# Kernel tuning notes

Hardware: AMD Instinct MI355X
Metric: run time of the kernel (lower is better)

Reference implementation:

```python
import jax, jax.numpy as jnp
import numpy as np

NUM_HEADS = 16
ROPE_THETA = 10000.0


def _rope_tables(S, d_k):
    # angles[s, j] = s / theta^(2j/d_k), j over d_k/2 pairs
    inv_freq = 1.0 / (ROPE_THETA ** (jnp.arange(0, d_k, 2, dtype=jnp.float32) / d_k))
    angles = jnp.arange(S, dtype=jnp.float32)[:, None] * inv_freq[None, :]  # [S, d_k/2]
    # repeat_interleave(…, 2, dim=-1) -> [S, d_k]
    cos2 = jnp.repeat(jnp.cos(angles), 2, axis=-1)
    sin2 = jnp.repeat(jnp.sin(angles), 2, axis=-1)
    return cos2, sin2


def _rotate_half(x):
    x_even = x[..., 0::2]
    x_odd = x[..., 1::2]
    return jnp.stack([-x_odd, x_even], axis=-1).reshape(x.shape)


def _apply_rope(x, cos2, sin2):
    # x: [B, H, S, d_k]; cos2/sin2: [S, d_k] broadcast over B, H
    return x * cos2 + _rotate_half(x) * sin2


def setup_inputs() -> dict:
    key = jax.random.key(0)
    k1, k2, k3, k4, k5 = jax.random.split(key, 5)
    B, S, D = 2, 2048, 1024
    std = (2.0 / (D + D)) ** 0.5
    x = jax.random.normal(k1, (B, S, D), dtype=jnp.float32)
    Wq = jax.random.normal(k2, (D, D), dtype=jnp.float32) * std
    Wk = jax.random.normal(k3, (D, D), dtype=jnp.float32) * std
    Wv = jax.random.normal(k4, (D, D), dtype=jnp.float32) * std
    Wo = jax.random.normal(k5, (D, D), dtype=jnp.float32) * std
    return {"x": x, "Wq": Wq, "Wk": Wk, "Wv": Wv, "Wo": Wo}


def reference(x, Wq, Wk, Wv, Wo):
    B, S, D = x.shape
    H = NUM_HEADS
    d_k = D // H
    # Linear is y = W x with W[d_out, d_in]
    Q = jnp.einsum('bsd,ed->bse', x, Wq).reshape(B, S, H, d_k).transpose(0, 2, 1, 3)
    K = jnp.einsum('bsd,ed->bse', x, Wk).reshape(B, S, H, d_k).transpose(0, 2, 1, 3)
    V = jnp.einsum('bsd,ed->bse', x, Wv).reshape(B, S, H, d_k).transpose(0, 2, 1, 3)
    cos2, sin2 = _rope_tables(S, d_k)
    Q = _apply_rope(Q, cos2, sin2)
    K = _apply_rope(K, cos2, sin2)
    scores = jnp.einsum('bhqd,bhkd->bhqk', Q, K) / jnp.sqrt(jnp.float32(d_k))
    causal = jnp.tril(jnp.ones((S, S), dtype=bool))
    scores = jnp.where(causal, scores, -jnp.inf)
    attn = jax.nn.softmax(scores, axis=-1)
    out = jnp.einsum('bhqk,bhkd->bhqd', attn, V)  # [B,H,S,d_k]
    out = out.transpose(0, 2, 1, 3).reshape(B, S, D)
    return jnp.einsum('bsd,ed->bse', out, Wo)
```

## Files before the change

kernel.cpp:

```cpp
#include <hip/hip_runtime.h>
#include <hip/hip_bf16.h>

typedef float f32x4 __attribute__((ext_vector_type(4)));
typedef __bf16 bf16x8 __attribute__((ext_vector_type(8)));

static constexpr int S  = 2048;
static constexpr int D  = 1024;
static constexpr int DK = 64;
static constexpr int KDIM = 1024;

#define AS1 __attribute__((address_space(1)))
#define AS3 __attribute__((address_space(3)))

__device__ __forceinline__ void glds16(const void* g, void* l) {
  __builtin_amdgcn_global_load_lds((const AS1 void*)g, (AS3 void*)l, 16, 0, 0);
}

__device__ __forceinline__ unsigned cvtpk(float lo, float hi) {
  unsigned r;
  asm("v_cvt_pk_bf16_f32 %0, %1, %2" : "=v"(r) : "v"(lo), "v"(hi));
  return r;
}

__device__ __forceinline__ void pl32swap(unsigned& a, unsigned& b) {
  asm("v_permlane32_swap_b32 %0, %1" : "+v"(a), "+v"(b));
}

__device__ __forceinline__ int kperm64(int k) {
  const int kf = k >> 4, hs = (k >> 2) & 3, r = k & 3;
  const bool inl = ((kf & 1) == (hs >> 1));
  const int h = inl ? hs : (hs ^ 2);
  const int j = inl ? r : (r + 4);
  return ((kf >> 1) << 5) + (h << 3) + j;
}

__global__ __launch_bounds__(256) void pre_kernel(
    const float* __restrict__ x,  const float* __restrict__ Wq,
    const float* __restrict__ Wk, const float* __restrict__ Wv,
    const float* __restrict__ Wo,
    __hip_bfloat16* __restrict__ xb, __hip_bfloat16* __restrict__ Wcat,
    __hip_bfloat16* __restrict__ Wob,
    float* __restrict__ cosT, float* __restrict__ sinT) {
  const int gid = blockIdx.x * 256 + threadIdx.x;
  if (gid < 2097152) {
    const float* src;
    __hip_bfloat16* dst;
    int off;
    if (gid < 1048576)      { src = x;  dst = xb;                  off = gid; }
    else if (gid < 1310720) { src = Wq; dst = Wcat;                off = gid - 1048576; }
    else if (gid < 1572864) { src = Wk; dst = Wcat + 1048576;      off = gid - 1310720; }
    else if (gid < 1835008) { src = Wv; dst = Wcat + 2097152;      off = gid - 1572864; }
    else                    { src = Wo; dst = Wob;                 off = gid - 1835008; }
    float4 v = reinterpret_cast<const float4*>(src)[off];
    union { ushort4 u; __hip_bfloat16 h[4]; } o;
    o.h[0] = __float2bfloat16(v.x);
    o.h[1] = __float2bfloat16(v.y);
    o.h[2] = __float2bfloat16(v.z);
    o.h[3] = __float2bfloat16(v.w);
    reinterpret_cast<ushort4*>(dst)[off] = o.u;
  } else {
    const int idx = gid - 2097152;
    const int s = idx >> 5, fi = idx & 31;
    float invf = powf(10000.0f, -(float)(2 * fi) / 64.0f);
    float ang = (float)s * invf;
    cosT[idx] = cosf(ang);
    sinT[idx] = sinf(ang);
  }
}

template <int MODE>
__global__ __launch_bounds__(256) void gemm_nt_kernel(
    const __hip_bfloat16* __restrict__ A,
    const __hip_bfloat16* __restrict__ Bw,
    float* __restrict__ Cf,
    __hip_bfloat16* __restrict__ Qr,
    __hip_bfloat16* __restrict__ Kr,
    __hip_bfloat16* __restrict__ Vt,
    const float* __restrict__ cosT,
    const float* __restrict__ sinT,
    int Ncols) {
  __shared__ __attribute__((aligned(16))) __hip_bfloat16 Asm[128 * 32];
  __shared__ __attribute__((aligned(16))) __hip_bfloat16 Bsm[128 * 32];
  const int tid = threadIdx.x;
  const int nbn = Ncols >> 7;
  const int cpx = gridDim.x >> 3;
  const int swz = (blockIdx.x & 7) * cpx + (blockIdx.x >> 3);
  const int bm = swz / nbn;
  const int bn = swz % nbn;
  const int m0 = bm << 7, n0 = bn << 7;
  const int lane = tid & 63;
  const int wid = tid >> 6;
  const int wm = wid >> 1, wn = wid & 1;
  const int r16 = lane & 15, hf = lane >> 4;

  f32x4 acc[4][4];
#pragma unroll
  for (int i = 0; i < 4; ++i)
#pragma unroll
    for (int j = 0; j < 4; ++j) acc[i][j] = (f32x4)0.0f;

  for (int k0 = 0; k0 < KDIM; k0 += 32) {
    __syncthreads();
#pragma unroll
    for (int i = 0; i < 2; ++i) {
      const int idx = i * 256 + tid;
      const int row = idx >> 2;
      const int cb = (idx & 3) << 4;
      glds16((const char*)A + ((size_t)(m0 + row) * KDIM + k0) * 2 + cb,
             (char*)Asm + idx * 16);
      glds16((const char*)Bw + ((size_t)(n0 + row) * KDIM + k0) * 2 + cb,
             (char*)Bsm + idx * 16);
    }
    __syncthreads();
    bf16x8 af[4], bfr[4];
#pragma unroll
    for (int mi = 0; mi < 4; ++mi)
      af[mi] = *(const bf16x8*)((const char*)Asm +
                                ((wm << 6) + (mi << 4) + r16) * 64 + hf * 16);
#pragma unroll
    for (int ni = 0; ni < 4; ++ni)
      bfr[ni] = *(const bf16x8*)((const char*)Bsm +
                                 ((wn << 6) + (ni << 4) + r16) * 64 + hf * 16);
#pragma unroll
    for (int mi = 0; mi < 4; ++mi)
#pragma unroll
      for (int ni = 0; ni < 4; ++ni)
        acc[mi][ni] = __builtin_amdgcn_mfma_f32_16x16x32_bf16(af[mi], bfr[ni],
                                                              acc[mi][ni], 0, 0, 0);
  }

  if constexpr (MODE == 0) {
#pragma unroll
    for (int mi = 0; mi < 4; ++mi) {
      const int rowb = m0 + (wm << 6) + (mi << 4) + (hf << 2);
#pragma unroll
      for (int ni = 0; ni < 4; ++ni) {
        const int col = n0 + (wn << 6) + (ni << 4) + r16;
#pragma unroll
        for (int r = 0; r < 4; ++r)
          Cf[(size_t)(rowb + r) * Ncols + col] = acc[mi][ni][r];
      }
    }
  } else {
    const int proj = n0 >> 10;
#pragma unroll
    for (int mi = 0; mi < 4; ++mi) {
      const int rowb = m0 + (wm << 6) + (mi << 4) + (hf << 2);
#pragma unroll
      for (int ni = 0; ni < 4; ++ni) {
        const int col = n0 + (wn << 6) + (ni << 4) + r16;
        const int ecol = col & 1023;
        const int h = ecol >> 6, dk = ecol & 63;
#pragma unroll
        for (int r = 0; r < 4; ++r) {
          float v = acc[mi][ni][r];
          const int row = rowb + r;
          const int b = row >> 11, s = row & 2047;
          if (proj < 2) {
            float p = __shfl_xor(v, 1, 64);
            const int fi = dk >> 1;
            const float c = cosT[(s << 5) + fi];
            const float sn = sinT[(s << 5) + fi];
            const float ov = v * c + ((dk & 1) ? p : -p) * sn;
            __hip_bfloat16* dst = (proj == 0) ? Qr : Kr;
            dst[((size_t)((b << 4) + h) * S + s) * DK + dk] = __float2bfloat16(ov);
          } else {
            const int sp = (s & ~63) | kperm64(s & 63);
            Vt[((size_t)((b << 4) + h) * DK + dk) * S + sp] = __float2bfloat16(v);
          }
        }
      }
    }
  }
}

__global__ __launch_bounds__(256) void attn_kernel(
    const __hip_bfloat16* __restrict__ Q,
    const __hip_bfloat16* __restrict__ Kr,
    const __hip_bfloat16* __restrict__ Vp,
    __hip_bfloat16* __restrict__ AO,
    __hip_bfloat16* __restrict__ Opart,
    float* __restrict__ ml) {
  __shared__ __attribute__((aligned(16))) __hip_bfloat16 Ks[2][64 * 64];
  __shared__ __attribute__((aligned(16))) __hip_bfloat16 Vs[2][64 * 64];
  const int tid = threadIdx.x;
  const int lane = tid & 63, wid = tid >> 6;
  const int r16 = lane & 15, hf = lane >> 4;
  const bool hi32 = (lane >= 32);
  const int bh = blockIdx.x & 31;
  const int item = blockIdx.x >> 5;
  const int g = item / 3, j = item - 3 * g;
  int qt, k0, k1;
  bool dosplit;
  if (j < 2) {
    qt = 15 - g;
    const int nt = (qt << 1) + 2;
    k0 = j ? (nt >> 1) : 0;
    k1 = j ? nt : (nt >> 1);
    dosplit = true;
  } else {
    qt = 7 - g;
    k0 = 0;
    k1 = (qt << 1) + 2;
    dosplit = false;
  }
  const __hip_bfloat16* Qh = Q + (size_t)bh * S * DK;
  const __hip_bfloat16* Kh = Kr + (size_t)bh * S * DK;
  const __hip_bfloat16* Vh = Vp + (size_t)bh * DK * S;

  const int qbase = (qt << 7) + (wid << 5);

  bf16x8 bq[2][2];
#pragma unroll
  for (int qf = 0; qf < 2; ++qf)
#pragma unroll
    for (int ks = 0; ks < 2; ++ks)
      bq[qf][ks] = *(const bf16x8*)(Qh + (size_t)(qbase + (qf << 4) + r16) * DK +
                                    ks * 32 + hf * 8);

  f32x4 o[2][4];
#pragma unroll
  for (int qf = 0; qf < 2; ++qf)
#pragma unroll
    for (int f = 0; f < 4; ++f) o[qf][f] = (f32x4)0.0f;
  float m[2] = {-1e30f, -1e30f}, l[2] = {0.0f, 0.0f};

#define STAGE(bufi, t)                                                         \
  {                                                                            \
    _Pragma("unroll") for (int i = 0; i < 2; ++i) {                            \
      const int idx = i * 256 + tid;                                           \
      const int row = idx >> 3;                                                \
      const int cb = (idx & 7) << 4;                                           \
      const int scb = cb ^ ((row & 7) << 4);                                   \
      glds16((const char*)Kh + ((size_t)(((t) << 6) + row) * DK) * 2 + scb,    \
             (char*)(&Ks[bufi][0]) + idx * 16);                                \
      glds16((const char*)Vh + ((size_t)row * S + ((t) << 6)) * 2 + scb,       \
             (char*)(&Vs[bufi][0]) + idx * 16);                                \
    }                                                                          \
  }

  STAGE(0, k0);
  __syncthreads();

  for (int kt = k0; kt < k1; ++kt) {
    const int cur = (kt - k0) & 1;
    if (kt + 1 < k1) STAGE(cur ^ 1, kt + 1);

    f32x4 p[2][4];
#pragma unroll
    for (int qf = 0; qf < 2; ++qf)
#pragma unroll
      for (int kf = 0; kf < 4; ++kf) p[qf][kf] = (f32x4)0.0f;
    __builtin_amdgcn_s_setprio(1);
#pragma unroll
    for (int ks = 0; ks < 2; ++ks) {
#pragma unroll
      for (int kf = 0; kf < 4; ++kf) {
        const int krow = (kf << 4) + r16;
        const int cb = (ks << 6) + (hf << 4);
        const bf16x8 ak = *(const bf16x8*)((const char*)(&Ks[cur][0]) +
                                           krow * 128 + (cb ^ ((krow & 7) << 4)));
#pragma unroll
        for (int qf = 0; qf < 2; ++qf)
          p[qf][kf] = __builtin_amdgcn_mfma_f32_16x16x32_bf16(ak, bq[qf][ks],
                                                              p[qf][kf], 0, 0, 0);
      }
    }
    __builtin_amdgcn_s_setprio(0);

    const bool diag = (kt >= (qt << 1));
#pragma unroll
    for (int qf = 0; qf < 2; ++qf) {
      const int qg = qbase + (qf << 4) + r16;
#pragma unroll
      for (int kf = 0; kf < 4; ++kf)
#pragma unroll
        for (int r = 0; r < 4; ++r) {
          float sv = p[qf][kf][r] * 0.125f;
          if (diag) {
            const int kg = (kt << 6) + (kf << 4) + (hf << 2) + r;
            if (kg > qg) sv = -1e30f;
          }
          p[qf][kf][r] = sv;
        }
    }

    float scl[2];
#pragma unroll
    for (int qf = 0; qf < 2; ++qf) {
      float t = p[qf][0][0];
#pragma unroll
      for (int kf = 0; kf < 4; ++kf)
#pragma unroll
        for (int r = 0; r < 4; ++r) t = fmaxf(t, p[qf][kf][r]);
      t = fmaxf(t, __shfl_xor(t, 16, 64));
      t = fmaxf(t, __shfl_xor(t, 32, 64));
      const float mn = fmaxf(m[qf], t);
      scl[qf] = __expf(m[qf] - mn);
      m[qf] = mn;
      float ss = 0.0f;
#pragma unroll
      for (int kf = 0; kf < 4; ++kf)
#pragma unroll
        for (int r = 0; r < 4; ++r) {
          const float e = __expf(p[qf][kf][r] - mn);
          p[qf][kf][r] = e;
          ss += e;
        }
      ss += __shfl_xor(ss, 16, 64);
      ss += __shfl_xor(ss, 32, 64);
      l[qf] = l[qf] * scl[qf] + ss;
#pragma unroll
      for (int f = 0; f < 4; ++f)
#pragma unroll
        for (int r = 0; r < 4; ++r) o[qf][f][r] *= scl[qf];
    }

    union PW { unsigned u[4]; bf16x8 v; };
    PW pb[2][2];
#pragma unroll
    for (int qf = 0; qf < 2; ++qf) {
      unsigned w[4][2];
#pragma unroll
      for (int kf = 0; kf < 4; ++kf) {
        w[kf][0] = cvtpk(p[qf][kf][0], p[qf][kf][1]);
        w[kf][1] = cvtpk(p[qf][kf][2], p[qf][kf][3]);
      }
#pragma unroll
      for (int ks = 0; ks < 2; ++ks) {
        unsigned a0 = w[2 * ks][0], b0 = w[2 * ks + 1][0];
        unsigned a1 = w[2 * ks][1], b1 = w[2 * ks + 1][1];
        pb[qf][ks].u[0] = hi32 ? b0 : a0;
        pb[qf][ks].u[1] = hi32 ? b1 : a1;
        pl32swap(a0, b0);
        pl32swap(a1, b1);
        pb[qf][ks].u[2] = hi32 ? a0 : b0;
        pb[qf][ks].u[3] = hi32 ? a1 : b1;
      }
    }

    __builtin_amdgcn_s_setprio(1);
#pragma unroll
    for (int ks = 0; ks < 2; ++ks) {
#pragma unroll
      for (int f = 0; f < 4; ++f) {
        const int vrow = (f << 4) + r16;
        const int cb = (ks << 6) + (hf << 4);
        const bf16x8 av = *(const bf16x8*)((const char*)(&Vs[cur][0]) +
                                           vrow * 128 + (cb ^ ((vrow & 7) << 4)));
#pragma unroll
        for (int qf = 0; qf < 2; ++qf)
          o[qf][f] = __builtin_amdgcn_mfma_f32_16x16x32_bf16(av, pb[qf][ks].v,
                                                             o[qf][f], 0, 0, 0);
      }
    }
    __builtin_amdgcn_s_setprio(0);

    __syncthreads();
  }
#undef STAGE

  if (!dosplit) {
    const int b = bh >> 4, h = bh & 15;
#pragma unroll
    for (int qf = 0; qf < 2; ++qf) {
      const float inv = 1.0f / l[qf];
      const int q = qbase + (qf << 4) + r16;
#pragma unroll
      for (int f = 0; f < 4; ++f)
#pragma unroll
        for (int r = 0; r < 4; ++r) {
          const int dv = (f << 4) + (hf << 2) + r;
          AO[((size_t)b * S + q) * D + (h << 6) + dv] =
              __float2bfloat16(o[qf][f][r] * inv);
        }
    }
  } else {
    const int sidx = (g << 1) | j;
    __hip_bfloat16* op = Opart + (((size_t)bh * 16 + sidx) << 13);
    float* mlp = ml + (((size_t)bh * 16 + sidx) << 8);
#pragma unroll
    for (int qf = 0; qf < 2; ++qf) {
      const float inv = 1.0f / l[qf];
      const int rowin = (wid << 5) + (qf << 4) + r16;
#pragma unroll
      for (int f = 0; f < 4; ++f)
#pragma unroll
        for (int r = 0; r < 4; ++r) {
          const int dv = (f << 4) + (hf << 2) + r;
          op[rowin * 64 + dv] = __float2bfloat16(o[qf][f][r] * inv);
        }
      if (hf == 0) {
        mlp[rowin * 2] = m[qf];
        mlp[rowin * 2 + 1] = l[qf];
      }
    }
  }
}

__global__ __launch_bounds__(256) void merge_kernel(
    const __hip_bfloat16* __restrict__ Opart,
    const float* __restrict__ ml,
    __hip_bfloat16* __restrict__ AO) {
  const int rg = blockIdx.x * 256 + threadIdx.x;
  const int bh = rg >> 10;
  const int rem = rg & 1023;
  const int gq = rem >> 7;
  const int rowin = rem & 127;
  const int s0 = bh * 16 + (gq << 1), s1 = s0 + 1;
  const float m0 = ml[(s0 << 8) + rowin * 2], l0 = ml[(s0 << 8) + rowin * 2 + 1];
  const float m1 = ml[(s1 << 8) + rowin * 2], l1 = ml[(s1 << 8) + rowin * 2 + 1];
  const float mx = fmaxf(m0, m1);
  float w0 = l0 * __expf(m0 - mx), w1 = l1 * __expf(m1 - mx);
  const float inv = 1.0f / (w0 + w1);
  w0 *= inv;
  w1 *= inv;
  const bf16x8* p0 = (const bf16x8*)(Opart + (((size_t)s0) << 13) + rowin * 64);
  const bf16x8* p1 = (const bf16x8*)(Opart + (((size_t)s1) << 13) + rowin * 64);
  const int b = bh >> 4, h = bh & 15;
  const int q = ((15 - gq) << 7) + rowin;
  bf16x8* dst = (bf16x8*)(AO + ((size_t)b * S + q) * D + (h << 6));
#pragma unroll
  for (int i = 0; i < 8; ++i) {
    bf16x8 a = p0[i], c = p1[i];
    bf16x8 r;
#pragma unroll
    for (int e = 0; e < 8; ++e)
      r[e] = (__bf16)(w0 * (float)a[e] + w1 * (float)c[e]);
    dst[i] = r;
  }
}

extern "C" void kernel_launch(void* const* d_in, const int* in_sizes, int n_in,
                              void* d_out, int out_size, void* d_ws, size_t ws_size,
                              hipStream_t stream) {
  (void)in_sizes; (void)n_in; (void)out_size; (void)ws_size;
  const float* x  = (const float*)d_in[0];
  const float* Wq = (const float*)d_in[1];
  const float* Wk = (const float*)d_in[2];
  const float* Wv = (const float*)d_in[3];
  const float* Wo = (const float*)d_in[4];
  float* out = (float*)d_out;
  char* ws = (char*)d_ws;
  const size_t MB = (size_t)1 << 20;
  __hip_bfloat16* xb   = (__hip_bfloat16*)(ws);
  __hip_bfloat16* Wcat = (__hip_bfloat16*)(ws + 8 * MB);
  __hip_bfloat16* Wob  = (__hip_bfloat16*)(ws + 14 * MB);
  __hip_bfloat16* Qr   = (__hip_bfloat16*)(ws + 16 * MB);
  __hip_bfloat16* Kr   = (__hip_bfloat16*)(ws + 24 * MB);
  __hip_bfloat16* Vt   = (__hip_bfloat16*)(ws + 32 * MB);
  __hip_bfloat16* AO   = (__hip_bfloat16*)(ws + 40 * MB);
  float* cosT = (float*)(ws + 48 * MB);
  float* sinT = (float*)(ws + 48 * MB + 256 * 1024);
  __hip_bfloat16* Opart = (__hip_bfloat16*)(ws);
  float* mlbuf = (float*)(ws + 8 * MB);

  pre_kernel<<<8448, 256, 0, stream>>>(x, Wq, Wk, Wv, Wo, xb, Wcat, Wob,
                                       cosT, sinT);
  gemm_nt_kernel<1><<<(4096 / 128) * (3072 / 128), 256, 0, stream>>>(
      xb, Wcat, nullptr, Qr, Kr, Vt, cosT, sinT, 3072);
  attn_kernel<<<32 * 24, 256, 0, stream>>>(Qr, Kr, Vt, AO, Opart, mlbuf);
  merge_kernel<<<128, 256, 0, stream>>>(Opart, mlbuf, AO);
  gemm_nt_kernel<0><<<(4096 / 128) * (1024 / 128), 256, 0, stream>>>(
      AO, Wob, out, nullptr, nullptr, nullptr, nullptr, nullptr, 1024);
}
```

Baseline: 221.6 us.

## Fold softmax scale into Q, use exp2 with lazy rescale, vectorize V stores, remap blocks

Q is pre-multiplied by 0.125*log2(e) in the projection epilogue, so attention can use the raw v_exp_f32 instead of __expf and skip the per-element score scaling. The online softmax now rescales O and l only when the running max grows by more than 8 (in log2 units), which removes most rescale multiplies at some cost in numerical headroom. V transpose stores are packed into 4-element vector writes, and attention blocks are reassigned through a lookup table to balance causal work across compute units. The masking is applied only on diagonal tiles, and the merge kernel switches to exp2 to match the new log2-domain max.

```diff
diff --git a/kernel.cpp b/kernel.cpp
--- a/kernel.cpp
+++ b/kernel.cpp
@@ -8,6 +8,7 @@
 static constexpr int D  = 1024;
 static constexpr int DK = 64;
 static constexpr int KDIM = 1024;
+static constexpr float QSCALE = 0.18033688f;
 
 #define AS1 __attribute__((address_space(1)))
 #define AS3 __attribute__((address_space(3)))
@@ -24,6 +25,12 @@
 
 __device__ __forceinline__ void pl32swap(unsigned& a, unsigned& b) {
   asm("v_permlane32_swap_b32 %0, %1" : "+v"(a), "+v"(b));
+}
+
+__device__ __forceinline__ float fexp2(float x) {
+  float r;
+  asm("v_exp_f32 %0, %1" : "=v"(r) : "v"(x));
+  return r;
 }
 
 __device__ __forceinline__ int kperm64(int k) {
@@ -46,11 +53,11 @@
     const float* src;
     __hip_bfloat16* dst;
     int off;
-    if (gid < 1048576)      { src = x;  dst = xb;                  off = gid; }
-    else if (gid < 1310720) { src = Wq; dst = Wcat;                off = gid - 1048576; }
-    else if (gid < 1572864) { src = Wk; dst = Wcat + 1048576;      off = gid - 1310720; }
-    else if (gid < 1835008) { src = Wv; dst = Wcat + 2097152;      off = gid - 1572864; }
-    else                    { src = Wo; dst = Wob;                 off = gid - 1835008; }
+    if (gid < 1048576)      { src = x;  dst = xb;             off = gid; }
+    else if (gid < 1310720) { src = Wq; dst = Wcat;           off = gid - 1048576; }
+    else if (gid < 1572864) { src = Wk; dst = Wcat + 1048576; off = gid - 1310720; }
+    else if (gid < 1835008) { src = Wv; dst = Wcat + 2097152; off = gid - 1572864; }
+    else                    { src = Wo; dst = Wob;            off = gid - 1835008; }
     float4 v = reinterpret_cast<const float4*>(src)[off];
     union { ushort4 u; __hip_bfloat16 h[4]; } o;
     o.h[0] = __float2bfloat16(v.x);
@@ -146,28 +153,35 @@
 #pragma unroll
     for (int mi = 0; mi < 4; ++mi) {
       const int rowb = m0 + (wm << 6) + (mi << 4) + (hf << 2);
+      const int b = rowb >> 11;
+      const int sbase = rowb & 2047;
 #pragma unroll
       for (int ni = 0; ni < 4; ++ni) {
         const int col = n0 + (wn << 6) + (ni << 4) + r16;
         const int ecol = col & 1023;
         const int h = ecol >> 6, dk = ecol & 63;
-#pragma unroll
-        for (int r = 0; r < 4; ++r) {
-          float v = acc[mi][ni][r];
-          const int row = rowb + r;
-          const int b = row >> 11, s = row & 2047;
-          if (proj < 2) {
+        if (proj < 2) {
+#pragma unroll
+          for (int r = 0; r < 4; ++r) {
+            float v = acc[mi][ni][r];
+            const int s = sbase + r;
             float p = __shfl_xor(v, 1, 64);
             const int fi = dk >> 1;
             const float c = cosT[(s << 5) + fi];
             const float sn = sinT[(s << 5) + fi];
-            const float ov = v * c + ((dk & 1) ? p : -p) * sn;
+            float ov = v * c + ((dk & 1) ? p : -p) * sn;
+            if (proj == 0) ov *= QSCALE;
             __hip_bfloat16* dst = (proj == 0) ? Qr : Kr;
             dst[((size_t)((b << 4) + h) * S + s) * DK + dk] = __float2bfloat16(ov);
-          } else {
-            const int sp = (s & ~63) | kperm64(s & 63);
-            Vt[((size_t)((b << 4) + h) * DK + dk) * S + sp] = __float2bfloat16(v);
           }
+        } else {
+          const int sp0 = (sbase & ~63) | kperm64(sbase & 63);
+          union { ushort4 u; __hip_bfloat16 hh[4]; } vp;
+#pragma unroll
+          for (int r = 0; r < 4; ++r)
+            vp.hh[r] = __float2bfloat16(acc[mi][ni][r]);
+          *reinterpret_cast<ushort4*>(
+              &Vt[((size_t)((b << 4) + h) * DK + dk) * S + sp0]) = vp.u;
         }
       }
     }
@@ -183,12 +197,16 @@
     float* __restrict__ ml) {
   __shared__ __attribute__((aligned(16))) __hip_bfloat16 Ks[2][64 * 64];
   __shared__ __attribute__((aligned(16))) __hip_bfloat16 Vs[2][64 * 64];
+  static const int T[8][3] = {{0, 1, 23},  {2, 5, 20},  {3, 9, 17}, {4, 15, 14},
+                              {6, 16, 21}, {7, 11, 18}, {10, 8, 22}, {12, 13, 19}};
   const int tid = threadIdx.x;
   const int lane = tid & 63, wid = tid >> 6;
   const int r16 = lane & 15, hf = lane >> 4;
   const bool hi32 = (lane >= 32);
   const int bh = blockIdx.x & 31;
-  const int item = blockIdx.x >> 5;
+  const int cg = (blockIdx.x >> 5) & 7;
+  const int slot = blockIdx.x >> 8;
+  const int item = T[cg][slot];
   const int g = item / 3, j = item - 3 * g;
   int qt, k0, k1;
   bool dosplit;
@@ -268,52 +286,51 @@
     }
     __builtin_amdgcn_s_setprio(0);
 
-    const bool diag = (kt >= (qt << 1));
+    if (kt >= (qt << 1)) {
+#pragma unroll
+      for (int qf = 0; qf < 2; ++qf) {
+        const int qg = qbase + (qf << 4) + r16;
+#pragma unroll
+        for (int kf = 0; kf < 4; ++kf)
+#pragma unroll
+          for (int r = 0; r < 4; ++r) {
+            const int kg = (kt << 6) + (kf << 4) + (hf << 2) + r;
+            if (kg > qg) p[qf][kf][r] = -1e30f;
+          }
+      }
+    }
+
 #pragma unroll
     for (int qf = 0; qf < 2; ++qf) {
-      const int qg = qbase + (qf << 4) + r16;
-#pragma unroll
-      for (int kf = 0; kf < 4; ++kf)
-#pragma unroll
-        for (int r = 0; r < 4; ++r) {
-          float sv = p[qf][kf][r] * 0.125f;
-          if (diag) {
-            const int kg = (kt << 6) + (kf << 4) + (hf << 2) + r;
-            if (kg > qg) sv = -1e30f;
-          }
-          p[qf][kf][r] = sv;
-        }
-    }
-
-    float scl[2];
-#pragma unroll
-    for (int qf = 0; qf < 2; ++qf) {
-      float t = p[qf][0][0];
-#pragma unroll
-      for (int kf = 0; kf < 4; ++kf)
-#pragma unroll
-        for (int r = 0; r < 4; ++r) t = fmaxf(t, p[qf][kf][r]);
+      f32x4 m4;
+#pragma unroll
+      for (int e = 0; e < 4; ++e)
+        m4[e] = fmaxf(fmaxf(p[qf][0][e], p[qf][1][e]),
+                      fmaxf(p[qf][2][e], p[qf][3][e]));
+      float t = fmaxf(fmaxf(m4[0], m4[1]), fmaxf(m4[2], m4[3]));
       t = fmaxf(t, __shfl_xor(t, 16, 64));
       t = fmaxf(t, __shfl_xor(t, 32, 64));
-      const float mn = fmaxf(m[qf], t);
-      scl[qf] = __expf(m[qf] - mn);
-      m[qf] = mn;
+      if (t > m[qf] + 8.0f) {
+        const float scl = fexp2(m[qf] - t);
+        m[qf] = t;
+        l[qf] *= scl;
+#pragma unroll
+        for (int f = 0; f < 4; ++f)
+#pragma unroll
+          for (int r = 0; r < 4; ++r) o[qf][f][r] *= scl;
+      }
       float ss = 0.0f;
 #pragma unroll
       for (int kf = 0; kf < 4; ++kf)
 #pragma unroll
         for (int r = 0; r < 4; ++r) {
-          const float e = __expf(p[qf][kf][r] - mn);
+          const float e = fexp2(p[qf][kf][r] - m[qf]);
           p[qf][kf][r] = e;
           ss += e;
         }
       ss += __shfl_xor(ss, 16, 64);
       ss += __shfl_xor(ss, 32, 64);
-      l[qf] = l[qf] * scl[qf] + ss;
-#pragma unroll
-      for (int f = 0; f < 4; ++f)
-#pragma unroll
-        for (int r = 0; r < 4; ++r) o[qf][f][r] *= scl[qf];
+      l[qf] += ss;
     }
 
     union PW { unsigned u[4]; bf16x8 v; };
@@ -411,7 +428,7 @@
   const float m0 = ml[(s0 << 8) + rowin * 2], l0 = ml[(s0 << 8) + rowin * 2 + 1];
   const float m1 = ml[(s1 << 8) + rowin * 2], l1 = ml[(s1 << 8) + rowin * 2 + 1];
   const float mx = fmaxf(m0, m1);
-  float w0 = l0 * __expf(m0 - mx), w1 = l1 * __expf(m1 - mx);
+  float w0 = l0 * fexp2(m0 - mx), w1 = l1 * fexp2(m1 - mx);
   const float inv = 1.0f / (w0 + w1);
   w0 *= inv;
   w1 *= inv;
```

After: 217.9 us. Within noise of the previous version (-1.7%).
